# Performance work log

Hardware: AMD Instinct MI355X
Metric: run time of the kernel (lower is better)

Reference implementation:

```python
import jax, jax.numpy as jnp
import numpy as np

B, C, H, W = 2, 256, 48, 48
NUM_HEADS = 8
HEAD_DIM = C // NUM_HEADS
SCALE = HEAD_DIM ** (-0.5)


def setup_inputs() -> dict:
    key = jax.random.key(0)
    ks = jax.random.split(key, 5)
    s = 1.0 / np.sqrt(C)  # conv1x1 fan-in scaling
    return {
        "x": jax.random.normal(ks[0], (B, C, H, W), jnp.float32),
        "Wq": jax.random.normal(ks[1], (C, C), jnp.float32) * s,
        "bq": jnp.zeros((C,), jnp.float32),
        "Wk": jax.random.normal(ks[2], (C, C), jnp.float32) * s,
        "bk": jnp.zeros((C,), jnp.float32),
        "Wv": jax.random.normal(ks[3], (C, C), jnp.float32) * s,
        "bv": jnp.zeros((C,), jnp.float32),
        "Wo": jax.random.normal(ks[4], (C, C), jnp.float32) * s,
        "bo": jnp.zeros((C,), jnp.float32),
    }


def _proj(x, Wf, bf):
    # conv1x1: [B,C,H,W] x [Cout,Cin] -> [B,Cout,H,W]
    return jnp.einsum('bchw,oc->bohw', x, Wf) + bf[None, :, None, None]


def reference(x, Wq, bq, Wk, bk, Wv, bv, Wo, bo):
    b, c, h, w = x.shape
    n = h * w
    # projections then split heads: [B, heads, N, head_dim]
    def to_heads(t):
        return t.reshape(b, NUM_HEADS, HEAD_DIM, n).transpose(0, 1, 3, 2)
    q = to_heads(_proj(x, Wq, bq))
    k = to_heads(_proj(x, Wk, bk))
    v = to_heads(_proj(x, Wv, bv))
    attn = jnp.einsum('bhnd,bhmd->bhnm', q, k) * SCALE
    attn = jax.nn.softmax(attn, axis=-1)  # max-subtract + softmax (stable)
    out = jnp.einsum('bhnm,bhmd->bhnd', attn, v)
    out = out.transpose(0, 1, 3, 2).reshape(b, c, h, w)
    return _proj(out, Wo, bo)
```

## Files before the change

### kernel.cpp

```cpp
#include <hip/hip_runtime.h>
#include <hip/hip_bf16.h>

#define BATCH 2
#define CH 256
#define NH 8
#define HD 32
#define NPOS 2304
#define SCALE 0.17677669529663687f
#define QSCALE 0.25503482f
#define NSPLIT 3
#define KSPAN (NPOS / NSPLIT)
#define NT (KSPAN / 128)
#define QT (NPOS / 16)

typedef __attribute__((ext_vector_type(8))) short short8;
typedef __attribute__((ext_vector_type(4))) short short4e;
typedef __attribute__((ext_vector_type(4))) float f32x4;
typedef __attribute__((ext_vector_type(4))) unsigned int u32x4;

__device__ __forceinline__ unsigned short f2bf(float f) {
    unsigned int u = __builtin_bit_cast(unsigned int, f);
    u += 0x7FFFu + ((u >> 16) & 1u);
    return (unsigned short)(u >> 16);
}

__device__ __forceinline__ unsigned int cvt_pk_bf16(float a, float b) {
    unsigned int r;
    asm("v_cvt_pk_bf16_f32 %0, %1, %2" : "=v"(r) : "v"(a), "v"(b));
    return r;
}

__device__ __forceinline__ float fast_exp2(float x) {
    float r;
    asm("v_exp_f32 %0, %1" : "=v"(r) : "v"(x));
    return r;
}

#define GLOAD_LDS16(gsrc, ldst) \
    __builtin_amdgcn_global_load_lds( \
        (const __attribute__((address_space(1))) void*)(gsrc), \
        (__attribute__((address_space(3))) void*)(ldst), 16, 0, 0)

__global__ __launch_bounds__(256) void convert_w(
    const float* __restrict__ Wq, const float* __restrict__ Wk,
    const float* __restrict__ Wv, const float* __restrict__ Wo,
    unsigned short* __restrict__ dst)
{
    int which = blockIdx.y;
    const float* src = (which == 0) ? Wq : (which == 1) ? Wk : (which == 2) ? Wv : Wo;
    unsigned short* d = dst + (size_t)which * CH * CH;
    int i = (blockIdx.x * 256 + threadIdx.x) * 4;
    f32x4 v = *(const f32x4*)&src[i];
    short4e o;
    #pragma unroll
    for (int j = 0; j < 4; ++j) o[j] = (short)f2bf(v[j]);
    *(short4e*)&d[i] = o;
}

__global__ __launch_bounds__(256) void transpose_x(
    const float* __restrict__ x, unsigned short* __restrict__ xT)
{
    int b = blockIdx.z, c0 = blockIdx.y * 32, n0 = blockIdx.x * 32;
    __shared__ float Ts[32][33];
    int t = threadIdx.x;
    int col = t & 31, row = t >> 5;
    #pragma unroll
    for (int i = 0; i < 4; ++i)
        Ts[row + i * 8][col] = x[((size_t)b * CH + c0 + row + i * 8) * NPOS + n0 + col];
    __syncthreads();
    #pragma unroll
    for (int i = 0; i < 4; ++i)
        xT[((size_t)b * NPOS + n0 + row + i * 8) * CH + c0 + col] = f2bf(Ts[col][row + i * 8]);
}

__global__ __launch_bounds__(256) void qkv_gemm(
    const unsigned short* __restrict__ xT,
    const unsigned short* __restrict__ Wb,
    const float* __restrict__ bq, const float* __restrict__ bk,
    const float* __restrict__ bv,
    unsigned short* __restrict__ qout, unsigned short* __restrict__ kout,
    unsigned short* __restrict__ vout)
{
    int b = blockIdx.z;
    int n0 = blockIdx.x * 64;
    int o0 = blockIdx.y * 64;
    int t = threadIdx.x, w = t >> 6, lane = t & 63;
    int lo = lane & 15, hi = lane >> 4;
    int ob = o0 + w * 16;

    const unsigned short* Wq = Wb;
    const unsigned short* Wk = Wb + (size_t)CH * CH;
    const unsigned short* Wv = Wb + (size_t)2 * CH * CH;
    const unsigned short* xb = xT + ((size_t)b * NPOS + n0) * CH;

    f32x4 aq[4] = {}, ak[4] = {}, av[4] = {};

    for (int k0 = 0; k0 < CH; k0 += 32) {
        short8 wqf = *(const short8*)&Wq[(size_t)(ob + lo) * CH + k0 + hi * 8];
        short8 wkf = *(const short8*)&Wk[(size_t)(ob + lo) * CH + k0 + hi * 8];
        short8 wvf = *(const short8*)&Wv[(size_t)(ob + lo) * CH + k0 + hi * 8];
        #pragma unroll
        for (int g = 0; g < 4; ++g) {
            short8 xf = *(const short8*)&xb[(size_t)(g * 16 + lo) * CH + k0 + hi * 8];
            aq[g] = __builtin_amdgcn_mfma_f32_16x16x32_bf16(wqf, xf, aq[g], 0, 0, 0);
            ak[g] = __builtin_amdgcn_mfma_f32_16x16x32_bf16(wkf, xf, ak[g], 0, 0, 0);
            av[g] = __builtin_amdgcn_mfma_f32_16x16x32_bf16(wvf, xf, av[g], 0, 0, 0);
        }
    }

    int h = ob >> 5;
    int olow = (ob & 31) + hi * 4;
    #pragma unroll
    for (int g = 0; g < 4; ++g) {
        int n = n0 + g * 16 + lo;
        size_t qkbase = ((size_t)(b * NH + h) * NPOS + n) * HD + olow;
        short4e pq, pk;
        #pragma unroll
        for (int r = 0; r < 4; ++r) {
            int o = ob + hi * 4 + r;
            pq[r] = (short)f2bf((aq[g][r] + bq[o]) * QSCALE);
            pk[r] = (short)f2bf(ak[g][r] + bk[o]);
        }
        *(short4e*)&qout[qkbase] = pq;
        *(short4e*)&kout[qkbase] = pk;

        int off = n & 127;
        int G = off >> 4;
        int his = lo >> 2, rr = lo & 3;
        int pi;
        if (G < 4) {
            pi = G * 32 + his * 8 + rr;
        } else {
            int gam = G & 3;
            pi = (his >= 2) ? (gam * 32 + (his - 2) * 8 + 4 + rr)
                            : ((gam ^ 1) * 32 + (his + 2) * 8 + 4 + rr);
        }
        int nperm = (n & ~127) | pi;
        size_t vbase = ((size_t)(b * NH + h) * HD + olow) * NPOS + nperm;
        #pragma unroll
        for (int r = 0; r < 4; ++r)
            vout[vbase + (size_t)r * NPOS] = f2bf(av[g][r] + bv[ob + hi * 4 + r]);
    }
}

__global__ __launch_bounds__(256) void attn_split(
    const unsigned short* __restrict__ Q,
    const unsigned short* __restrict__ K,
    const unsigned short* __restrict__ V,
    float* __restrict__ Opart,
    float* __restrict__ Lpart)
{
    const int N = NPOS;
    int xb_ = blockIdx.x;
    int bh = xb_ & 15;
    int split = xb_ >> 4;
    int w = threadIdx.x >> 6;
    int qt = blockIdx.y * 4 + w;
    int n0 = qt * 16;
    int lane = threadIdx.x & 63;
    int lo = lane & 15, hi = lane >> 4;
    bool upperhalf = lane >= 32;

    __shared__ unsigned short Ks[2][128 * HD];
    __shared__ unsigned short Vs[2][HD * 128];

    short8 qa = *(const short8*)(Q + ((size_t)bh * N + n0 + lo) * HD + hi * 8);

    const unsigned short* Kb = K + (size_t)bh * N * HD;
    const unsigned short* Vb = V + (size_t)bh * HD * N;

    short8 ones;
    #pragma unroll
    for (int j = 0; j < 8; ++j) ones[j] = (short)0x3F80;

    f32x4 oacc[2] = {{0.f,0.f,0.f,0.f},{0.f,0.f,0.f,0.f}};
    f32x4 lacc = {0.f,0.f,0.f,0.f};

    const int kbeg = split * KSPAN;

    auto stage = [&](int b, int k0) {
        #pragma unroll
        for (int j = 0; j < 2; ++j) {
            int L = w * 128 + j * 64 + lane;
            int row = L >> 2, blk = L & 3;
            const unsigned short* src = Kb + (size_t)(k0 + row) * HD + (blk ^ (row & 3)) * 8;
            GLOAD_LDS16(src, &Ks[b][(size_t)(w * 128 + j * 64) * 8]);
        }
        #pragma unroll
        for (int j = 0; j < 2; ++j) {
            int L = w * 128 + j * 64 + lane;
            int row = L >> 4, blk = L & 15;
            const unsigned short* src = Vb + (size_t)row * N + k0 + (blk ^ (row & 15)) * 8;
            GLOAD_LDS16(src, &Vs[b][(size_t)(w * 128 + j * 64) * 8]);
        }
    };

    stage(0, kbeg);
    __syncthreads();

    int buf = 0;
    #pragma unroll
    for (int kt = 0; kt < NT; ++kt) {
        int k0 = kbeg + kt * 128;
        if (kt + 1 < NT) stage(buf ^ 1, k0 + 128);

        f32x4 s[8];
        __builtin_amdgcn_s_setprio(1);
        #pragma unroll
        for (int g = 0; g < 8; ++g) {
            short8 kf = *(const short8*)&Ks[buf][(g * 16 + lo) * HD + (hi ^ (lo & 3)) * 8];
            s[g] = __builtin_amdgcn_mfma_f32_16x16x32_bf16(kf, qa, (f32x4){0.f,0.f,0.f,0.f}, 0, 0, 0);
        }
        __builtin_amdgcn_s_setprio(0);

        #pragma unroll
        for (int g = 0; g < 8; ++g)
            #pragma unroll
            for (int r = 0; r < 4; ++r)
                s[g][r] = fast_exp2(s[g][r]);

        unsigned int pk0[8], pk1[8];
        #pragma unroll
        for (int g = 0; g < 8; ++g) {
            pk0[g] = cvt_pk_bf16(s[g][0], s[g][1]);
            pk1[g] = cvt_pk_bf16(s[g][2], s[g][3]);
        }

        #pragma unroll
        for (int c = 0; c < 4; ++c) {
            unsigned int z0 = upperhalf ? pk0[4 + c] : pk0[4 + (c ^ 1)];
            unsigned int z1 = upperhalf ? pk1[4 + c] : pk1[4 + (c ^ 1)];
            unsigned int r0 = (unsigned int)__shfl_xor((int)z0, 32);
            unsigned int r1 = (unsigned int)__shfl_xor((int)z1, 32);
            u32x4 fv = {pk0[c], pk1[c], r0, r1};
            short8 frag = __builtin_bit_cast(short8, fv);

            __builtin_amdgcn_s_setprio(1);
            lacc = __builtin_amdgcn_mfma_f32_16x16x32_bf16(frag, ones, lacc, 0, 0, 0);
            #pragma unroll
            for (int df = 0; df < 2; ++df) {
                short8 vf = *(const short8*)&Vs[buf][(df * 16 + lo) * 128 + ((c * 4 + hi) ^ lo) * 8];
                oacc[df] = __builtin_amdgcn_mfma_f32_16x16x32_bf16(frag, vf, oacc[df], 0, 0, 0);
            }
            __builtin_amdgcn_s_setprio(0);
        }

        __syncthreads();
        buf ^= 1;
    }

    size_t tidx  = (((size_t)bh * QT + qt) * NSPLIT + split);
    float* ob = Opart + tidx * (HD * 16);
    #pragma unroll
    for (int df = 0; df < 2; ++df)
        *(f32x4*)&ob[(df * 16 + lo) * 16 + hi * 4] = oacc[df];
    if (lo == 0) {
        float* lb = Lpart + tidx * 16;
        #pragma unroll
        for (int r = 0; r < 4; ++r) lb[hi * 4 + r] = lacc[r];
    }
}

__global__ __launch_bounds__(256) void attn_merge(
    const float* __restrict__ Opart,
    const float* __restrict__ Lpart,
    unsigned short* __restrict__ omT)
{
    int bh = blockIdx.y, b = bh >> 3, h = bh & 7;
    int qt = blockIdx.x, n0 = qt * 16;
    int t = threadIdx.x;
    int d = t & 31;
    int r0 = t >> 5;
    size_t base = ((size_t)bh * QT + qt) * NSPLIT;
    #pragma unroll
    for (int i = 0; i < 2; ++i) {
        int row = r0 + i * 8;
        float osum = 0.f, lsum = 0.f;
        #pragma unroll
        for (int s = 0; s < NSPLIT; ++s) {
            osum += Opart[(base + s) * (HD * 16) + d * 16 + row];
            lsum += Lpart[(base + s) * 16 + row];
        }
        omT[((size_t)b * NPOS + n0 + row) * CH + h * HD + d] = f2bf(osum / lsum);
    }
}

__global__ __launch_bounds__(256) void wo_gemm(
    const unsigned short* __restrict__ omT,
    const unsigned short* __restrict__ Wo,
    const float* __restrict__ bo,
    float* __restrict__ out)
{
    int b = blockIdx.z;
    int n0 = blockIdx.x * 64;
    int o0 = blockIdx.y * 64;
    int t = threadIdx.x, w = t >> 6, lane = t & 63;
    int lo = lane & 15, hi = lane >> 4;
    int ob = o0 + w * 16;

    const unsigned short* xb = omT + ((size_t)b * NPOS + n0) * CH;

    f32x4 acc[4] = {};
    for (int k0 = 0; k0 < CH; k0 += 32) {
        short8 wf = *(const short8*)&Wo[(size_t)(ob + lo) * CH + k0 + hi * 8];
        #pragma unroll
        for (int g = 0; g < 4; ++g) {
            short8 xf = *(const short8*)&xb[(size_t)(g * 16 + lo) * CH + k0 + hi * 8];
            acc[g] = __builtin_amdgcn_mfma_f32_16x16x32_bf16(wf, xf, acc[g], 0, 0, 0);
        }
    }

    #pragma unroll
    for (int g = 0; g < 4; ++g) {
        int n = n0 + g * 16 + lo;
        #pragma unroll
        for (int r = 0; r < 4; ++r) {
            int o = ob + hi * 4 + r;
            out[((size_t)b * CH + o) * NPOS + n] = acc[g][r] + bo[o];
        }
    }
}

extern "C" void kernel_launch(void* const* d_in, const int* in_sizes, int n_in,
                              void* d_out, int out_size, void* d_ws, size_t ws_size,
                              hipStream_t stream) {
    const float* x  = (const float*)d_in[0];
    const float* Wq = (const float*)d_in[1];
    const float* bq = (const float*)d_in[2];
    const float* Wk = (const float*)d_in[3];
    const float* bk = (const float*)d_in[4];
    const float* Wv = (const float*)d_in[5];
    const float* bv = (const float*)d_in[6];
    const float* Wo = (const float*)d_in[7];
    const float* bo = (const float*)d_in[8];
    float* out = (float*)d_out;

    const size_t E  = (size_t)BATCH * CH * NPOS;
    const size_t WS = (size_t)CH * CH;
    unsigned short* wbf = (unsigned short*)d_ws;
    unsigned short* xT  = wbf + 4 * WS;
    unsigned short* qb  = xT + E;
    unsigned short* kb  = qb + E;
    unsigned short* vT  = kb + E;
    float* Opart = (float*)(vT + E);
    float* Lpart = Opart + (size_t)16 * QT * NSPLIT * (HD * 16);
    unsigned short* om = xT;
    (void)ws_size; (void)in_sizes; (void)n_in; (void)out_size;

    hipLaunchKernelGGL(convert_w, dim3(64, 4), dim3(256), 0, stream,
                       Wq, Wk, Wv, Wo, wbf);
    hipLaunchKernelGGL(transpose_x, dim3(NPOS / 32, CH / 32, BATCH), dim3(256), 0, stream,
                       x, xT);
    hipLaunchKernelGGL(qkv_gemm, dim3(NPOS / 64, CH / 64, BATCH), dim3(256), 0, stream,
                       xT, wbf, bq, bk, bv, qb, kb, vT);
    hipLaunchKernelGGL(attn_split, dim3(NSPLIT * 16, QT / 4), dim3(256), 0, stream,
                       qb, kb, vT, Opart, Lpart);
    hipLaunchKernelGGL(attn_merge, dim3(QT, BATCH * NH), dim3(256), 0, stream,
                       Opart, Lpart, om);
    hipLaunchKernelGGL(wo_gemm, dim3(NPOS / 64, CH / 64, BATCH), dim3(256), 0, stream,
                       om, wbf + 3 * WS, bo, out);
}
```

Baseline: 75.76 us.

## Fuse weight conversion with x transpose and halve GEMM output tiles

Merges the weight bf16 conversion and the x transpose into one prep kernel, saving a launch. The QKV and Wo GEMMs now use 32-output-channel tiles with waves split 2x2 over channels and positions, which doubles the grid for better CU occupancy but adds redundant x loads per block. In the attention kernel, the raised wave priority now spans the whole PV loop instead of being toggled on each iteration.

Result: faster. 71.31 us (-5.9%).

```diff
diff --git a/kernel.cpp b/kernel.cpp
--- a/kernel.cpp
+++ b/kernel.cpp
@@ -41,36 +41,40 @@
         (const __attribute__((address_space(1))) void*)(gsrc), \
         (__attribute__((address_space(3))) void*)(ldst), 16, 0, 0)
 
-__global__ __launch_bounds__(256) void convert_w(
+__global__ __launch_bounds__(256) void prep(
     const float* __restrict__ Wq, const float* __restrict__ Wk,
     const float* __restrict__ Wv, const float* __restrict__ Wo,
-    unsigned short* __restrict__ dst)
-{
-    int which = blockIdx.y;
-    const float* src = (which == 0) ? Wq : (which == 1) ? Wk : (which == 2) ? Wv : Wo;
-    unsigned short* d = dst + (size_t)which * CH * CH;
-    int i = (blockIdx.x * 256 + threadIdx.x) * 4;
-    f32x4 v = *(const f32x4*)&src[i];
-    short4e o;
-    #pragma unroll
-    for (int j = 0; j < 4; ++j) o[j] = (short)f2bf(v[j]);
-    *(short4e*)&d[i] = o;
-}
-
-__global__ __launch_bounds__(256) void transpose_x(
-    const float* __restrict__ x, unsigned short* __restrict__ xT)
-{
-    int b = blockIdx.z, c0 = blockIdx.y * 32, n0 = blockIdx.x * 32;
+    const float* __restrict__ x,
+    unsigned short* __restrict__ wbf, unsigned short* __restrict__ xT)
+{
     __shared__ float Ts[32][33];
+    int id = blockIdx.x;
     int t = threadIdx.x;
-    int col = t & 31, row = t >> 5;
-    #pragma unroll
-    for (int i = 0; i < 4; ++i)
-        Ts[row + i * 8][col] = x[((size_t)b * CH + c0 + row + i * 8) * NPOS + n0 + col];
-    __syncthreads();
-    #pragma unroll
-    for (int i = 0; i < 4; ++i)
-        xT[((size_t)b * NPOS + n0 + row + i * 8) * CH + c0 + col] = f2bf(Ts[col][row + i * 8]);
+    if (id < 256) {
+        int which = id >> 6;
+        const float* src = (which == 0) ? Wq : (which == 1) ? Wk : (which == 2) ? Wv : Wo;
+        unsigned short* d = wbf + (size_t)which * CH * CH;
+        int i = ((id & 63) * 256 + t) * 4;
+        f32x4 v = *(const f32x4*)&src[i];
+        short4e o;
+        #pragma unroll
+        for (int j = 0; j < 4; ++j) o[j] = (short)f2bf(v[j]);
+        *(short4e*)&d[i] = o;
+    } else {
+        int tid = id - 256;
+        int b = tid / 576;
+        int rem = tid % 576;
+        int c0 = (rem / 72) * 32;
+        int n0 = (rem % 72) * 32;
+        int col = t & 31, row = t >> 5;
+        #pragma unroll
+        for (int i = 0; i < 4; ++i)
+            Ts[row + i * 8][col] = x[((size_t)b * CH + c0 + row + i * 8) * NPOS + n0 + col];
+        __syncthreads();
+        #pragma unroll
+        for (int i = 0; i < 4; ++i)
+            xT[((size_t)b * NPOS + n0 + row + i * 8) * CH + c0 + col] = f2bf(Ts[col][row + i * 8]);
+    }
 }
 
 __global__ __launch_bounds__(256) void qkv_gemm(
@@ -83,24 +87,25 @@
 {
     int b = blockIdx.z;
     int n0 = blockIdx.x * 64;
-    int o0 = blockIdx.y * 64;
+    int o0 = blockIdx.y * 32;
     int t = threadIdx.x, w = t >> 6, lane = t & 63;
     int lo = lane & 15, hi = lane >> 4;
-    int ob = o0 + w * 16;
+    int ob = o0 + (w & 1) * 16;
+    int nb = n0 + (w >> 1) * 32;
 
     const unsigned short* Wq = Wb;
     const unsigned short* Wk = Wb + (size_t)CH * CH;
     const unsigned short* Wv = Wb + (size_t)2 * CH * CH;
-    const unsigned short* xb = xT + ((size_t)b * NPOS + n0) * CH;
-
-    f32x4 aq[4] = {}, ak[4] = {}, av[4] = {};
+    const unsigned short* xb = xT + ((size_t)b * NPOS + nb) * CH;
+
+    f32x4 aq[2] = {}, ak[2] = {}, av[2] = {};
 
     for (int k0 = 0; k0 < CH; k0 += 32) {
         short8 wqf = *(const short8*)&Wq[(size_t)(ob + lo) * CH + k0 + hi * 8];
         short8 wkf = *(const short8*)&Wk[(size_t)(ob + lo) * CH + k0 + hi * 8];
         short8 wvf = *(const short8*)&Wv[(size_t)(ob + lo) * CH + k0 + hi * 8];
         #pragma unroll
-        for (int g = 0; g < 4; ++g) {
+        for (int g = 0; g < 2; ++g) {
             short8 xf = *(const short8*)&xb[(size_t)(g * 16 + lo) * CH + k0 + hi * 8];
             aq[g] = __builtin_amdgcn_mfma_f32_16x16x32_bf16(wqf, xf, aq[g], 0, 0, 0);
             ak[g] = __builtin_amdgcn_mfma_f32_16x16x32_bf16(wkf, xf, ak[g], 0, 0, 0);
@@ -111,8 +116,8 @@
     int h = ob >> 5;
     int olow = (ob & 31) + hi * 4;
     #pragma unroll
-    for (int g = 0; g < 4; ++g) {
-        int n = n0 + g * 16 + lo;
+    for (int g = 0; g < 2; ++g) {
+        int n = nb + g * 16 + lo;
         size_t qkbase = ((size_t)(b * NH + h) * NPOS + n) * HD + olow;
         short4e pq, pk;
         #pragma unroll
@@ -226,6 +231,7 @@
             pk1[g] = cvt_pk_bf16(s[g][2], s[g][3]);
         }
 
+        __builtin_amdgcn_s_setprio(1);
         #pragma unroll
         for (int c = 0; c < 4; ++c) {
             unsigned int z0 = upperhalf ? pk0[4 + c] : pk0[4 + (c ^ 1)];
@@ -235,15 +241,14 @@
             u32x4 fv = {pk0[c], pk1[c], r0, r1};
             short8 frag = __builtin_bit_cast(short8, fv);
 
-            __builtin_amdgcn_s_setprio(1);
             lacc = __builtin_amdgcn_mfma_f32_16x16x32_bf16(frag, ones, lacc, 0, 0, 0);
             #pragma unroll
             for (int df = 0; df < 2; ++df) {
                 short8 vf = *(const short8*)&Vs[buf][(df * 16 + lo) * 128 + ((c * 4 + hi) ^ lo) * 8];
                 oacc[df] = __builtin_amdgcn_mfma_f32_16x16x32_bf16(frag, vf, oacc[df], 0, 0, 0);
             }
-            __builtin_amdgcn_s_setprio(0);
-        }
+        }
+        __builtin_amdgcn_s_setprio(0);
 
         __syncthreads();
         buf ^= 1;
@@ -293,26 +298,27 @@
 {
     int b = blockIdx.z;
     int n0 = blockIdx.x * 64;
-    int o0 = blockIdx.y * 64;
+    int o0 = blockIdx.y * 32;
     int t = threadIdx.x, w = t >> 6, lane = t & 63;
     int lo = lane & 15, hi = lane >> 4;
-    int ob = o0 + w * 16;
-
-    const unsigned short* xb = omT + ((size_t)b * NPOS + n0) * CH;
-
-    f32x4 acc[4] = {};
+    int ob = o0 + (w & 1) * 16;
+    int nb = n0 + (w >> 1) * 32;
+
+    const unsigned short* xb = omT + ((size_t)b * NPOS + nb) * CH;
+
+    f32x4 acc[2] = {};
     for (int k0 = 0; k0 < CH; k0 += 32) {
         short8 wf = *(const short8*)&Wo[(size_t)(ob + lo) * CH + k0 + hi * 8];
         #pragma unroll
-        for (int g = 0; g < 4; ++g) {
+        for (int g = 0; g < 2; ++g) {
             short8 xf = *(const short8*)&xb[(size_t)(g * 16 + lo) * CH + k0 + hi * 8];
             acc[g] = __builtin_amdgcn_mfma_f32_16x16x32_bf16(wf, xf, acc[g], 0, 0, 0);
         }
     }
 
     #pragma unroll
-    for (int g = 0; g < 4; ++g) {
-        int n = n0 + g * 16 + lo;
+    for (int g = 0; g < 2; ++g) {
+        int n = nb + g * 16 + lo;
         #pragma unroll
         for (int r = 0; r < 4; ++r) {
             int o = ob + hi * 4 + r;
@@ -347,16 +353,14 @@
     unsigned short* om = xT;
     (void)ws_size; (void)in_sizes; (void)n_in; (void)out_size;
 
-    hipLaunchKernelGGL(convert_w, dim3(64, 4), dim3(256), 0, stream,
-                       Wq, Wk, Wv, Wo, wbf);
-    hipLaunchKernelGGL(transpose_x, dim3(NPOS / 32, CH / 32, BATCH), dim3(256), 0, stream,
-                       x, xT);
-    hipLaunchKernelGGL(qkv_gemm, dim3(NPOS / 64, CH / 64, BATCH), dim3(256), 0, stream,
+    hipLaunchKernelGGL(prep, dim3(256 + 1152), dim3(256), 0, stream,
+                       Wq, Wk, Wv, Wo, x, wbf, xT);
+    hipLaunchKernelGGL(qkv_gemm, dim3(NPOS / 64, CH / 32, BATCH), dim3(256), 0, stream,
                        xT, wbf, bq, bk, bv, qb, kb, vT);
     hipLaunchKernelGGL(attn_split, dim3(NSPLIT * 16, QT / 4), dim3(256), 0, stream,
                        qb, kb, vT, Opart, Lpart);
     hipLaunchKernelGGL(attn_merge, dim3(QT, BATCH * NH), dim3(256), 0, stream,
                        Opart, Lpart, om);
-    hipLaunchKernelGGL(wo_gemm, dim3(NPOS / 64, CH / 64, BATCH), dim3(256), 0, stream,
+    hipLaunchKernelGGL(wo_gemm, dim3(NPOS / 64, CH / 32, BATCH), dim3(256), 0, stream,
                        om, wbf + 3 * WS, bo, out);
 }
```
